# Performance work log

Measured on AMD Instinct MI355X. Metric: run time of the kernel, lower is better.

## Reference

```python
import jax, jax.numpy as jnp
import numpy as np

H = 8      # head count
ES = 96    # per-head dim
EMB = H * ES
L = 6      # layers
B, T = 8, 512
LN_EPS = 1e-5

def _layernorm(x, g, b):
    mu = jnp.mean(x, axis=-1, keepdims=True)
    var = jnp.mean(jnp.square(x - mu), axis=-1, keepdims=True)
    return (x - mu) * jax.lax.rsqrt(var + LN_EPS) * g + b

def setup_inputs() -> dict:
    key = jax.random.key(0)
    ks = jax.random.split(key, 6)
    s = 0.02
    return {
        "x": jax.random.normal(ks[0], (B, T, EMB), jnp.float32),
        "Wkqv": jax.random.normal(ks[1], (L, 3 * ES, ES), jnp.float32) * s,
        "Wproj": jax.random.normal(ks[2], (L, EMB, EMB), jnp.float32) * s,
        "ln1_g": jnp.ones((L, EMB), jnp.float32),
        "ln1_b": jnp.zeros((L, EMB), jnp.float32),
        "ln2_g": jnp.ones((L, EMB), jnp.float32),
        "ln2_b": jnp.zeros((L, EMB), jnp.float32),
        "ff_w1": jax.random.normal(ks[3], (L, 4 * EMB, EMB), jnp.float32) * s,
        "ff_b1": jnp.zeros((L, 4 * EMB), jnp.float32),
        "ff_w2": jax.random.normal(ks[4], (L, EMB, 4 * EMB), jnp.float32) * s,
        "ff_b2": jnp.zeros((L, EMB), jnp.float32),
    }

def _forward(x, Wkqv, Wproj, ln1_g, ln1_b, ln2_g, ln2_b, ff_w1, ff_b1, ff_w2, ff_b2):
    scale = 1.0 / jnp.sqrt(jnp.float32(ES))

    def step(carry, p):
        x, prev = carry
        wkqv, wproj, g1, b1, g2, b2, w1, bb1, w2, bb2 = p
        Bx, Tx, _ = x.shape
        xh = x.reshape(Bx, Tx, H, ES)                         # [B,T,H,es]
        kqv = jnp.einsum('bthe,fe->bthf', xh, wkqv)           # [B,T,H,3es]
        k, q, v = jnp.split(kqv, 3, axis=-1)                  # torch.split order: k,q,v
        # residual attention: raw scores + previous layer's raw scores
        score = jnp.einsum('bihk,bjhk->bijh', q, k) * scale + prev  # [B,T,T,H]
        att = jax.nn.softmax(score, axis=2)                   # over key axis j
        res = jnp.einsum('btih,bihs->bths', att, v).reshape(Bx, Tx, EMB)
        res = res @ wproj.T
        x = _layernorm(x + res, g1, b1)
        ff = jax.nn.gelu(x @ w1.T + bb1, approximate=False) @ w2.T + bb2
        x = _layernorm(x + ff, g2, b2)
        return (x, score), None

    prev0 = jnp.zeros((x.shape[0], x.shape[1], x.shape[1], H), x.dtype)
    (x, _), _ = jax.lax.scan(step, (x, prev0),
                             (Wkqv, Wproj, ln1_g, ln1_b, ln2_g, ln2_b,
                              ff_w1, ff_b1, ff_w2, ff_b2))
    return x

def reference(x, Wkqv, Wproj, ln1_g, ln1_b, ln2_g, ln2_b, ff_w1, ff_b1, ff_w2, ff_b2):
    return _forward(x, Wkqv, Wproj, ln1_g, ln1_b, ln2_g, ln2_b, ff_w1, ff_b1, ff_w2, ff_b2)
```

## Files before the change

### kernel.cpp

```cpp
#include <hip/hip_runtime.h>
#include <math.h>

#define BB 8
#define TT 512
#define HH 8
#define ESS 96
#define EMBD 768
#define FFD 3072
#define NLAYER 6
#define KHMAX 576

typedef unsigned short ushort_t;
typedef __attribute__((ext_vector_type(8))) short short8;
typedef __attribute__((ext_vector_type(4))) float f32x4;
typedef __attribute__((ext_vector_type(4))) unsigned short ushort4v;

static __device__ __forceinline__ ushort_t f2b(float f) {
    unsigned u = __builtin_bit_cast(unsigned, f);
    unsigned r = (u + 0x7fffu + ((u >> 16) & 1u)) >> 16;
    return (ushort_t)r;
}
static __device__ __forceinline__ float b2f(ushort_t u) {
    return __builtin_bit_cast(float, ((unsigned)u) << 16);
}

#define GLDS(gp, lp) __builtin_amdgcn_global_load_lds( \
    (const __attribute__((address_space(1))) void*)(gp), \
    (__attribute__((address_space(3))) void*)(lp), 16, 0, 0)

template<int BM, int BN, int WM, int WN, int OUTBF, int HASBIAS, int GELU, int BETA>
__global__ __launch_bounds__(256) void gemm_mfma(
    const ushort_t* __restrict__ A, int lda,
    const ushort_t* __restrict__ B, int ldb,
    void* __restrict__ Cv, int ldc,
    int K, float alpha,
    const float* __restrict__ bias,
    int bdiv, long sAb, long sAh, long sBb, long sBh, long sCb, long sCh)
{
    constexpr int BK = 32;
    constexpr int WTM = BM / WM;
    constexpr int WTN = BN / WN;
    constexpr int MF = WTM / 16, NF = WTN / 16;
    constexpr int ACH = (BM * BK * 2) / 1024;
    constexpr int BCH = (BN * BK * 2) / 1024;

    const int z = blockIdx.z;
    const int zb = z / bdiv, zh = z % bdiv;
    A += (long)zb * sAb + (long)zh * sAh;
    B += (long)zb * sBb + (long)zh * sBh;
    const long coff = (long)zb * sCb + (long)zh * sCh;

    __shared__ ushort_t As[BM * BK];
    __shared__ ushort_t Bs[BN * BK];

    const int tid = threadIdx.x;
    const int w = tid >> 6, lane = tid & 63;
    const int wr = w / WN, wc = w % WN;
    const int m0 = blockIdx.y * BM;
    const int n0 = blockIdx.x * BN;

    f32x4 acc[MF][NF] = {};

    const int fr = lane & 15;
    const int kb = lane >> 4;

    for (int k0 = 0; k0 < K; k0 += BK) {
#pragma unroll
        for (int q = 0; q < (ACH + 3) / 4; ++q) {
            int ci = q * 4 + w;
            if (ci < ACH) {
                int e = ci * 512 + lane * 8;
                int r = e >> 5, c = e & 31;
                GLDS(A + (long)(m0 + r) * lda + (k0 + c), (char*)As + ci * 1024);
            }
        }
#pragma unroll
        for (int q = 0; q < (BCH + 3) / 4; ++q) {
            int ci = q * 4 + w;
            if (ci < BCH) {
                int e = ci * 512 + lane * 8;
                int r = e >> 5, c = e & 31;
                GLDS(B + (long)(n0 + r) * ldb + (k0 + c), (char*)Bs + ci * 1024);
            }
        }
        __syncthreads();

        short8 af[MF], bfr[NF];
#pragma unroll
        for (int fm = 0; fm < MF; ++fm)
            af[fm] = *(const short8*)&As[(wr * WTM + fm * 16 + fr) * 32 + kb * 8];
#pragma unroll
        for (int fn = 0; fn < NF; ++fn)
            bfr[fn] = *(const short8*)&Bs[(wc * WTN + fn * 16 + fr) * 32 + kb * 8];
#pragma unroll
        for (int fm = 0; fm < MF; ++fm)
#pragma unroll
            for (int fn = 0; fn < NF; ++fn)
                acc[fm][fn] = __builtin_amdgcn_mfma_f32_16x16x32_bf16(
                    af[fm], bfr[fn], acc[fm][fn], 0, 0, 0);
        __syncthreads();
    }

    const int cr = lane >> 4;
    const int cc = lane & 15;
#pragma unroll
    for (int fm = 0; fm < MF; ++fm) {
#pragma unroll
        for (int fn = 0; fn < NF; ++fn) {
#pragma unroll
            for (int j = 0; j < 4; ++j) {
                int gm = m0 + wr * WTM + fm * 16 + cr * 4 + j;
                int gn = n0 + wc * WTN + fn * 16 + cc;
                float v = alpha * acc[fm][fn][j];
                if (HASBIAS) v += bias[gn];
                if (GELU) {
                    float zz = 1.5957691216f * fmaf(0.044715f * v * v, v, v);
                    v = v / (1.f + __expf(-zz));
                }
                long idx = coff + (long)gm * ldc + gn;
                if (BETA) v += ((const float*)Cv)[idx];
                if (OUTBF) ((ushort_t*)Cv)[idx] = f2b(v);
                else       ((float*)Cv)[idx] = v;
            }
        }
    }
}

__global__ __launch_bounds__(256) void kqv_gemm(
    const ushort_t* __restrict__ A,
    const ushort_t* __restrict__ Bw,
    ushort_t* __restrict__ Kh, ushort_t* __restrict__ Qh,
    ushort_t* __restrict__ Vt, int loff, float scale)
{
    constexpr int BM = 128, BN = 96, BK = 32;
    __shared__ ushort_t As[BM * BK];
    __shared__ ushort_t Bs[BN * BK];

    const int tid = threadIdx.x;
    const int w = tid >> 6, lane = tid & 63;
    const int m0 = blockIdx.y * BM;
    const int n0 = blockIdx.x * BN;

    f32x4 acc[2][6] = {};
    const int fr = lane & 15;
    const int kb = lane >> 4;

    for (int k0 = 0; k0 < 96; k0 += BK) {
#pragma unroll
        for (int q = 0; q < 2; ++q) {
            int ci = q * 4 + w;
            int e = ci * 512 + lane * 8;
            int r = e >> 5, c = e & 31;
            GLDS(A + (long)(m0 + r) * ESS + (k0 + c), (char*)As + ci * 1024);
        }
        {
            int ci = w;
            int e = ci * 512 + lane * 8;
            int r = e >> 5, c = e & 31;
            GLDS(Bw + (long)(n0 + r) * ESS + (k0 + c), (char*)Bs + ci * 1024);
            if (w < 2) {
                int ci2 = 4 + w;
                int e2 = ci2 * 512 + lane * 8;
                int r2 = e2 >> 5, c2 = e2 & 31;
                GLDS(Bw + (long)(n0 + r2) * ESS + (k0 + c2), (char*)Bs + ci2 * 1024);
            }
        }
        __syncthreads();

        short8 af[2], bfr[6];
#pragma unroll
        for (int fm = 0; fm < 2; ++fm)
            af[fm] = *(const short8*)&As[(w * 32 + fm * 16 + fr) * 32 + kb * 8];
#pragma unroll
        for (int fn = 0; fn < 6; ++fn)
            bfr[fn] = *(const short8*)&Bs[(fn * 16 + fr) * 32 + kb * 8];
#pragma unroll
        for (int fm = 0; fm < 2; ++fm)
#pragma unroll
            for (int fn = 0; fn < 6; ++fn)
                acc[fm][fn] = __builtin_amdgcn_mfma_f32_16x16x32_bf16(
                    af[fm], bfr[fn], acc[fm][fn], 0, 0, 0);
        __syncthreads();
    }

    const int cr = lane >> 4;
    const int cc = lane & 15;
    const int kind = blockIdx.x;
#pragma unroll
    for (int fm = 0; fm < 2; ++fm) {
#pragma unroll
        for (int fn = 0; fn < 6; ++fn) {
#pragma unroll
            for (int j = 0; j < 4; ++j) {
                int gm = m0 + w * 32 + fm * 16 + cr * 4 + j;
                int s = fn * 16 + cc;
                float v = acc[fm][fn][j];
                int h = gm & 7;
                int bt = gm >> 3;
                int t = bt & 511, b = bt >> 9;
                int bh = b * HH + h;
                if (kind == 0)
                    Kh[((long)(bh * TT + t)) * KHMAX + loff + s] = f2b(v);
                else if (kind == 1)
                    Qh[((long)(bh * TT + t)) * KHMAX + loff + s] = f2b(v * scale);
                else
                    Vt[((long)(bh * ESS + s)) * TT + t] = f2b(v);
            }
        }
    }
}

__global__ __launch_bounds__(256) void fused_attn(
    const ushort_t* __restrict__ Qh,
    const ushort_t* __restrict__ Kh,
    const ushort_t* __restrict__ Vt,
    ushort_t* __restrict__ attn,
    int Kd)
{
    __shared__ char lds[40960];
    ushort_t* As = (ushort_t*)lds;
    ushort_t* Bs = (ushort_t*)(lds + 2048);
    ushort_t* Pt = (ushort_t*)(lds + 2048);
    ushort_t* Vs = (ushort_t*)(lds + 34816);
    float* red   = (float*)(lds + 34816);
    float* red2  = (float*)(lds + 35328);

    const int wg = blockIdx.x;
    const int xcd = wg & 7;
    const int sub = wg >> 3;
    const int m0 = (sub & 15) * 32;
    const int bh = (sub >> 4) * 8 + xcd;
    const int b = bh >> 3, h = bh & 7;

    const int tid = threadIdx.x;
    const int w = tid >> 6, lane = tid & 63;
    const int fr = lane & 15, kb = lane >> 4;
    const int cr = kb, cc = fr;

    f32x4 acc[2][8] = {};

    for (int k0 = 0; k0 < Kd; k0 += 32) {
        if (w < 2) {
            int e = w * 512 + lane * 8;
            int r = e >> 5, c = e & 31;
            GLDS(Qh + ((long)(bh * TT + m0 + r)) * KHMAX + k0 + c,
                 (char*)As + w * 1024);
        }
#pragma unroll
        for (int q = 0; q < 8; ++q) {
            int ci = q * 4 + w;
            int e = ci * 512 + lane * 8;
            int r = e >> 5, c = e & 31;
            GLDS(Kh + ((long)(bh * TT + r)) * KHMAX + k0 + c,
                 (char*)Bs + ci * 1024);
        }
        __syncthreads();
        short8 af0 = *(const short8*)&As[fr * 32 + kb * 8];
        short8 af1 = *(const short8*)&As[(16 + fr) * 32 + kb * 8];
#pragma unroll
        for (int fn = 0; fn < 8; ++fn) {
            short8 bf = *(const short8*)&Bs[(w * 128 + fn * 16 + fr) * 32 + kb * 8];
            acc[0][fn] = __builtin_amdgcn_mfma_f32_16x16x32_bf16(af0, bf, acc[0][fn], 0, 0, 0);
            acc[1][fn] = __builtin_amdgcn_mfma_f32_16x16x32_bf16(af1, bf, acc[1][fn], 0, 0, 0);
        }
        __syncthreads();
    }

#pragma unroll
    for (int fm = 0; fm < 2; ++fm)
#pragma unroll
        for (int j = 0; j < 4; ++j) {
            float mx = -1e30f;
#pragma unroll
            for (int fn = 0; fn < 8; ++fn) mx = fmaxf(mx, acc[fm][fn][j]);
            for (int o = 1; o <= 8; o <<= 1) mx = fmaxf(mx, __shfl_xor(mx, o));
            if (cc == 0) red[w * 32 + fm * 16 + cr * 4 + j] = mx;
        }
    __syncthreads();

    float inv[2][4];
#pragma unroll
    for (int fm = 0; fm < 2; ++fm)
#pragma unroll
        for (int j = 0; j < 4; ++j) {
            int r = fm * 16 + cr * 4 + j;
            float mx = fmaxf(fmaxf(red[r], red[32 + r]), fmaxf(red[64 + r], red[96 + r]));
            float s = 0.f;
#pragma unroll
            for (int fn = 0; fn < 8; ++fn) {
                float e = __expf(acc[fm][fn][j] - mx);
                acc[fm][fn][j] = e;
                s += e;
            }
            for (int o = 1; o <= 8; o <<= 1) s += __shfl_xor(s, o);
            if (cc == 0) red2[w * 32 + r] = s;
        }
    __syncthreads();
#pragma unroll
    for (int fm = 0; fm < 2; ++fm)
#pragma unroll
        for (int j = 0; j < 4; ++j) {
            int r = fm * 16 + cr * 4 + j;
            inv[fm][j] = 1.f / (red2[r] + red2[32 + r] + red2[64 + r] + red2[96 + r]);
        }

#pragma unroll
    for (int fm = 0; fm < 2; ++fm)
#pragma unroll
        for (int fn = 0; fn < 8; ++fn)
#pragma unroll
            for (int j = 0; j < 4; ++j) {
                int row = fm * 16 + cr * 4 + j;
                int col = w * 128 + fn * 16 + cc;
                Pt[row * 512 + (col ^ ((row & 7) << 3))] = f2b(acc[fm][fn][j] * inv[fm][j]);
            }
    __syncthreads();

    const int wr = w >> 1, wc2 = w & 1;
    f32x4 po[3] = {};
    for (int j0 = 0; j0 < TT; j0 += 32) {
#pragma unroll
        for (int q = 0; q < 2; ++q) {
            int ci = q * 4 + w;
            if (ci < 6) {
                int e = ci * 512 + lane * 8;
                int r = e >> 5, c = e & 31;
                GLDS(Vt + ((long)(bh * ESS + r)) * TT + j0 + c, (char*)Vs + ci * 1024);
            }
        }
        __syncthreads();
        int prow = wr * 16 + fr;
        short8 pa = *(const short8*)&Pt[prow * 512 + ((j0 + kb * 8) ^ ((prow & 7) << 3))];
#pragma unroll
        for (int fn = 0; fn < 3; ++fn) {
            short8 vb = *(const short8*)&Vs[(wc2 * 48 + fn * 16 + fr) * 32 + kb * 8];
            po[fn] = __builtin_amdgcn_mfma_f32_16x16x32_bf16(pa, vb, po[fn], 0, 0, 0);
        }
        __syncthreads();
    }

#pragma unroll
    for (int fn = 0; fn < 3; ++fn)
#pragma unroll
        for (int j = 0; j < 4; ++j) {
            int grow = m0 + wr * 16 + cr * 4 + j;
            int gcol = h * ESS + wc2 * 48 + fn * 16 + cc;
            attn[((long)(b * TT + grow)) * EMBD + gcol] = f2b(po[fn][j]);
        }
}

__global__ __launch_bounds__(256) void cvt_f2b(
    const float* __restrict__ in, ushort_t* __restrict__ out)
{
    const int i = blockIdx.x * 256 + threadIdx.x;
    float4 v = ((const float4*)in)[i];
    ushort4v o = {f2b(v.x), f2b(v.y), f2b(v.z), f2b(v.w)};
    ((ushort4v*)out)[i] = o;
}

static __device__ __forceinline__ void cvt_w_one(
    int r, int layer,
    const float* Wkqv, const float* Wproj, const float* w1, const float* w2,
    ushort_t* dst_layer)
{
    const float* src; int base;
    if (r < 6912)        { src = Wkqv  + (long)layer * 27648;   base = 0; }
    else if (r < 154368) { src = Wproj + (long)layer * 589824;  base = 6912; }
    else if (r < 744192) { src = w1    + (long)layer * 2359296; base = 154368; }
    else                 { src = w2    + (long)layer * 2359296; base = 744192; }
    int j = r - base;
    float4 v = ((const float4*)src)[j];
    ushort4v o = {f2b(v.x), f2b(v.y), f2b(v.z), f2b(v.w)};
    ((ushort4v*)dst_layer)[r] = o;
}

__global__ __launch_bounds__(256) void cvt_weights_all(
    const float* __restrict__ Wkqv, const float* __restrict__ Wproj,
    const float* __restrict__ w1, const float* __restrict__ w2,
    ushort_t* __restrict__ dst)
{
    int i4 = blockIdx.x * 256 + threadIdx.x;
    int layer = i4 / 1334016;
    int r = i4 - layer * 1334016;
    cvt_w_one(r, layer, Wkqv, Wproj, w1, w2, dst + (long)layer * 5336064);
}

__global__ __launch_bounds__(256) void cvt_weights_layer(
    const float* __restrict__ Wkqv, const float* __restrict__ Wproj,
    const float* __restrict__ w1, const float* __restrict__ w2,
    ushort_t* __restrict__ dst, int layer)
{
    int r = blockIdx.x * 256 + threadIdx.x;
    cvt_w_one(r, layer, Wkqv, Wproj, w1, w2, dst);
}

template<int NR, int FINAL>
__global__ __launch_bounds__(192) void add_ln(
    ushort_t* __restrict__ xio, const ushort_t* __restrict__ res, long rstride,
    const float* __restrict__ bias,
    const float* __restrict__ g, const float* __restrict__ bta,
    float* __restrict__ xf)
{
    const long row = blockIdx.x;
    ushort4v* xr = (ushort4v*)(xio + row * EMBD);
    __shared__ float sh[4];
    const int tid = threadIdx.x;
    const int lane = tid & 63, w = tid >> 6;

    ushort4v xu = xr[tid];
    float v[4] = {b2f(xu.x), b2f(xu.y), b2f(xu.z), b2f(xu.w)};
#pragma unroll
    for (int p = 0; p < NR; ++p) {
        ushort4v u = ((const ushort4v*)(res + p * rstride + row * EMBD))[tid];
        v[0] += b2f(u.x); v[1] += b2f(u.y); v[2] += b2f(u.z); v[3] += b2f(u.w);
    }
    if (bias) {
        float4 b4 = ((const float4*)bias)[tid];
        v[0] += b4.x; v[1] += b4.y; v[2] += b4.z; v[3] += b4.w;
    }
    float s = v[0] + v[1] + v[2] + v[3];
    for (int o = 32; o; o >>= 1) s += __shfl_xor(s, o);
    if (lane == 0) sh[w] = s;
    __syncthreads();
    float mu = (sh[0] + sh[1] + sh[2]) * (1.f / EMBD);

    float var = 0.f;
#pragma unroll
    for (int c = 0; c < 4; ++c) { float d = v[c] - mu; var += d * d; }
    for (int o = 32; o; o >>= 1) var += __shfl_xor(var, o);
    __syncthreads();
    if (lane == 0) sh[w] = var;
    __syncthreads();
    var = (sh[0] + sh[1] + sh[2]) * (1.f / EMBD);
    float rstd = rsqrtf(var + 1e-5f);

    const float4 g4 = ((const float4*)g)[tid];
    const float4 b4 = ((const float4*)bta)[tid];
    float o0 = (v[0] - mu) * rstd * g4.x + b4.x;
    float o1 = (v[1] - mu) * rstd * g4.y + b4.y;
    float o2 = (v[2] - mu) * rstd * g4.z + b4.z;
    float o3 = (v[3] - mu) * rstd * g4.w + b4.w;
    ushort4v ob = {f2b(o0), f2b(o1), f2b(o2), f2b(o3)};
    xr[tid] = ob;
    if (FINAL) {
        float4 ov = {o0, o1, o2, o3};
        ((float4*)(xf + row * EMBD))[tid] = ov;
    }
}

extern "C" void kernel_launch(void* const* d_in, const int* in_sizes, int n_in,
                              void* d_out, int out_size, void* d_ws, size_t ws_size,
                              hipStream_t stream) {
    const float* x_in  = (const float*)d_in[0];
    const float* Wkqv  = (const float*)d_in[1];
    const float* Wproj = (const float*)d_in[2];
    const float* ln1_g = (const float*)d_in[3];
    const float* ln1_b = (const float*)d_in[4];
    const float* ln2_g = (const float*)d_in[5];
    const float* ln2_b = (const float*)d_in[6];
    const float* ff_w1 = (const float*)d_in[7];
    const float* ff_b1 = (const float*)d_in[8];
    const float* ff_w2 = (const float*)d_in[9];
    const float* ff_b2 = (const float*)d_in[10];

    float* xout = (float*)d_out;
    char* ws = (char*)d_ws;
    ushort_t* Qh     = (ushort_t*)(ws);
    ushort_t* Kh     = (ushort_t*)(ws + 37748736);
    ushort_t* Vtb    = (ushort_t*)(ws + 75497472);
    ushort_t* resb   = (ushort_t*)(ws + 75497472);
    ushort_t* h1b    = (ushort_t*)(ws + 100663296);
    ushort_t* xb     = (ushort_t*)(ws + 125829120);
    ushort_t* attnb  = (ushort_t*)(ws + 132120576);
    ushort_t* Wall   = (ushort_t*)(ws + 138412032);
    const size_t WLAYER_B = 10672128;
    const int    WLAYER_E = 5336064;
    const int big = (ws_size >= 138412032 + 6 * WLAYER_B) ? 1 : 0;
    const long RES_STRIDE = 3145728;

    cvt_f2b<<<3072, 256, 0, stream>>>(x_in, xb);
    if (big)
        cvt_weights_all<<<31266, 256, 0, stream>>>(Wkqv, Wproj, ff_w1, ff_w2, Wall);

    const float scale = 0.10206207261596577f;

    for (int l = 0; l < NLAYER; ++l) {
        const float* b1 = ff_b1 + (size_t)l * FFD;
        const float* b2 = ff_b2 + (size_t)l * EMBD;

        ushort_t* Wl = Wall + (big ? (long)l * WLAYER_E : 0);
        if (!big)
            cvt_weights_layer<<<5211, 256, 0, stream>>>(Wkqv, Wproj, ff_w1, ff_w2, Wl, l);
        ushort_t* Wkqvb  = Wl;
        ushort_t* Wprojb = Wl + 27648;
        ushort_t* W1b    = Wl + 617472;
        ushort_t* W2b    = Wl + 2976768;

        kqv_gemm<<<dim3(3, 256, 1), 256, 0, stream>>>(
            xb, Wkqvb, Kh, Qh, Vtb, l * ESS, scale);

        fused_attn<<<1024, 256, 0, stream>>>(
            Qh, Kh, Vtb, attnb, ESS * (l + 1));

        gemm_mfma<128, 128, 2, 2, 1, 0, 0, 0><<<dim3(6, 32, 2), 256, 0, stream>>>(
            attnb, EMBD, Wprojb, EMBD, resb, EMBD, EMBD / 2, 1.f, nullptr,
            1, 384, 0, 384, 0, RES_STRIDE, 0);

        add_ln<2, 0><<<BB * TT, 192, 0, stream>>>(xb, resb, RES_STRIDE, nullptr,
            ln1_g + (size_t)l * EMBD, ln1_b + (size_t)l * EMBD, nullptr);

        gemm_mfma<128, 128, 2, 2, 1, 1, 1, 0><<<dim3(24, 32, 1), 256, 0, stream>>>(
            xb, EMBD, W1b, EMBD, h1b, FFD, EMBD, 1.f, b1,
            1, 0, 0, 0, 0, 0, 0);

        gemm_mfma<128, 128, 2, 2, 1, 0, 0, 0><<<dim3(6, 32, 4), 256, 0, stream>>>(
            h1b, FFD, W2b, FFD, resb, EMBD, FFD / 4, 1.f, nullptr,
            1, 768, 0, 768, 0, RES_STRIDE, 0);

        if (l == NLAYER - 1)
            add_ln<4, 1><<<BB * TT, 192, 0, stream>>>(xb, resb, RES_STRIDE, b2,
                ln2_g + (size_t)l * EMBD, ln2_b + (size_t)l * EMBD, xout);
        else
            add_ln<4, 0><<<BB * TT, 192, 0, stream>>>(xb, resb, RES_STRIDE, b2,
                ln2_g + (size_t)l * EMBD, ln2_b + (size_t)l * EMBD, nullptr);
    }
}
```

Measured before the change: 1.074 ms.

## Process 64 query rows per attention workgroup with 8 waves sharing K tiles

The fused attention kernel now uses 512 threads and 64 query rows per block instead of 256 threads and 32 rows, halving the grid. The two 4-wave groups share each staged K tile, so global K loads per query row are halved. LDS usage grows to about 70KB, which lowers how many blocks fit per CU, and an extra barrier is added before P is written because P now aliases the K buffer.

```diff
diff --git a/kernel.cpp b/kernel.cpp
--- a/kernel.cpp
+++ b/kernel.cpp
@@ -210,56 +210,58 @@
     }
 }
 
-__global__ __launch_bounds__(256) void fused_attn(
+__global__ __launch_bounds__(512) void fused_attn(
     const ushort_t* __restrict__ Qh,
     const ushort_t* __restrict__ Kh,
     const ushort_t* __restrict__ Vt,
     ushort_t* __restrict__ attn,
     int Kd)
 {
-    __shared__ char lds[40960];
-    ushort_t* As = (ushort_t*)lds;
-    ushort_t* Bs = (ushort_t*)(lds + 2048);
-    ushort_t* Pt = (ushort_t*)(lds + 2048);
-    ushort_t* Vs = (ushort_t*)(lds + 34816);
-    float* red   = (float*)(lds + 34816);
-    float* red2  = (float*)(lds + 35328);
+    __shared__ char lds[71680];
+    ushort_t* Pt = (ushort_t*)lds;
+    ushort_t* Bs = (ushort_t*)lds;
+    ushort_t* As = (ushort_t*)(lds + 32768);
+    ushort_t* Vs = (ushort_t*)(lds + 65536);
+    float* red   = (float*)(lds + 65536);
+    float* red2  = (float*)(lds + 66560);
 
     const int wg = blockIdx.x;
     const int xcd = wg & 7;
     const int sub = wg >> 3;
-    const int m0 = (sub & 15) * 32;
-    const int bh = (sub >> 4) * 8 + xcd;
+    const int m0 = (sub & 7) * 64;
+    const int bh = (sub >> 3) * 8 + xcd;
     const int b = bh >> 3, h = bh & 7;
 
     const int tid = threadIdx.x;
     const int w = tid >> 6, lane = tid & 63;
+    const int g = w >> 2;
+    const int wg4 = w & 3;
     const int fr = lane & 15, kb = lane >> 4;
     const int cr = kb, cc = fr;
 
     f32x4 acc[2][8] = {};
 
     for (int k0 = 0; k0 < Kd; k0 += 32) {
-        if (w < 2) {
+        if (w < 4) {
             int e = w * 512 + lane * 8;
             int r = e >> 5, c = e & 31;
             GLDS(Qh + ((long)(bh * TT + m0 + r)) * KHMAX + k0 + c,
                  (char*)As + w * 1024);
         }
 #pragma unroll
-        for (int q = 0; q < 8; ++q) {
-            int ci = q * 4 + w;
+        for (int q = 0; q < 4; ++q) {
+            int ci = q * 8 + w;
             int e = ci * 512 + lane * 8;
             int r = e >> 5, c = e & 31;
             GLDS(Kh + ((long)(bh * TT + r)) * KHMAX + k0 + c,
                  (char*)Bs + ci * 1024);
         }
         __syncthreads();
-        short8 af0 = *(const short8*)&As[fr * 32 + kb * 8];
-        short8 af1 = *(const short8*)&As[(16 + fr) * 32 + kb * 8];
+        short8 af0 = *(const short8*)&As[(g * 32 + fr) * 32 + kb * 8];
+        short8 af1 = *(const short8*)&As[(g * 32 + 16 + fr) * 32 + kb * 8];
 #pragma unroll
         for (int fn = 0; fn < 8; ++fn) {
-            short8 bf = *(const short8*)&Bs[(w * 128 + fn * 16 + fr) * 32 + kb * 8];
+            short8 bf = *(const short8*)&Bs[(wg4 * 128 + fn * 16 + fr) * 32 + kb * 8];
             acc[0][fn] = __builtin_amdgcn_mfma_f32_16x16x32_bf16(af0, bf, acc[0][fn], 0, 0, 0);
             acc[1][fn] = __builtin_amdgcn_mfma_f32_16x16x32_bf16(af1, bf, acc[1][fn], 0, 0, 0);
         }
@@ -274,7 +276,7 @@
 #pragma unroll
             for (int fn = 0; fn < 8; ++fn) mx = fmaxf(mx, acc[fm][fn][j]);
             for (int o = 1; o <= 8; o <<= 1) mx = fmaxf(mx, __shfl_xor(mx, o));
-            if (cc == 0) red[w * 32 + fm * 16 + cr * 4 + j] = mx;
+            if (cc == 0) red[g * 128 + wg4 * 32 + fm * 16 + cr * 4 + j] = mx;
         }
     __syncthreads();
 
@@ -284,7 +286,8 @@
 #pragma unroll
         for (int j = 0; j < 4; ++j) {
             int r = fm * 16 + cr * 4 + j;
-            float mx = fmaxf(fmaxf(red[r], red[32 + r]), fmaxf(red[64 + r], red[96 + r]));
+            const float* rg = red + g * 128;
+            float mx = fmaxf(fmaxf(rg[r], rg[32 + r]), fmaxf(rg[64 + r], rg[96 + r]));
             float s = 0.f;
 #pragma unroll
             for (int fn = 0; fn < 8; ++fn) {
@@ -293,7 +296,7 @@
                 s += e;
             }
             for (int o = 1; o <= 8; o <<= 1) s += __shfl_xor(s, o);
-            if (cc == 0) red2[w * 32 + r] = s;
+            if (cc == 0) red2[g * 128 + wg4 * 32 + r] = s;
         }
     __syncthreads();
 #pragma unroll
@@ -301,8 +304,10 @@
 #pragma unroll
         for (int j = 0; j < 4; ++j) {
             int r = fm * 16 + cr * 4 + j;
-            inv[fm][j] = 1.f / (red2[r] + red2[32 + r] + red2[64 + r] + red2[96 + r]);
-        }
+            const float* rg = red2 + g * 128;
+            inv[fm][j] = 1.f / (rg[r] + rg[32 + r] + rg[64 + r] + rg[96 + r]);
+        }
+    __syncthreads();
 
 #pragma unroll
     for (int fm = 0; fm < 2; ++fm)
@@ -310,8 +315,8 @@
         for (int fn = 0; fn < 8; ++fn)
 #pragma unroll
             for (int j = 0; j < 4; ++j) {
-                int row = fm * 16 + cr * 4 + j;
-                int col = w * 128 + fn * 16 + cc;
+                int row = g * 32 + fm * 16 + cr * 4 + j;
+                int col = wg4 * 128 + fn * 16 + cc;
                 Pt[row * 512 + (col ^ ((row & 7) << 3))] = f2b(acc[fm][fn][j] * inv[fm][j]);
             }
     __syncthreads();
@@ -319,14 +324,10 @@
     const int wr = w >> 1, wc2 = w & 1;
     f32x4 po[3] = {};
     for (int j0 = 0; j0 < TT; j0 += 32) {
-#pragma unroll
-        for (int q = 0; q < 2; ++q) {
-            int ci = q * 4 + w;
-            if (ci < 6) {
-                int e = ci * 512 + lane * 8;
-                int r = e >> 5, c = e & 31;
-                GLDS(Vt + ((long)(bh * ESS + r)) * TT + j0 + c, (char*)Vs + ci * 1024);
-            }
+        if (w < 6) {
+            int e = w * 512 + lane * 8;
+            int r = e >> 5, c = e & 31;
+            GLDS(Vt + ((long)(bh * ESS + r)) * TT + j0 + c, (char*)Vs + w * 1024);
         }
         __syncthreads();
         int prow = wr * 16 + fr;
@@ -499,7 +500,7 @@
         kqv_gemm<<<dim3(3, 256, 1), 256, 0, stream>>>(
             xb, Wkqvb, Kh, Qh, Vtb, l * ESS, scale);
 
-        fused_attn<<<1024, 256, 0, stream>>>(
+        fused_attn<<<512, 512, 0, stream>>>(
             Qh, Kh, Vtb, attnb, ESS * (l + 1));
 
         gemm_mfma<128, 128, 2, 2, 1, 0, 0, 0><<<dim3(6, 32, 2), 256, 0, stream>>>(
```

After: 948.9 us (median of 2 runs). 11.6% less time.
